# Performance work log

Measured on AMD Instinct MI355X. Metric: run time of the kernel, lower is better.

The kernel has to match this reference:

```python
import jax, jax.numpy as jnp
import numpy as np

B, S, E = 2, 2048, 2048
H, D = 16, 128  # num_attention_heads, head_dim = hidden_size // num_heads


def rotate_half(x):
    x1 = x[..., : x.shape[-1] // 2]
    x2 = x[..., x.shape[-1] // 2 :]
    return jnp.concatenate((-x2, x1), axis=-1)


def setup_inputs() -> dict:
    key = jax.random.key(0)
    ks = jax.random.split(key, 7)
    return {
        "hidden_states": jax.random.normal(ks[0], (B, S, E), dtype=jnp.float32),
        "cos": jax.random.uniform(ks[1], (1, 1, S, D), dtype=jnp.float32),
        "sin": jax.random.uniform(ks[2], (1, 1, S, D), dtype=jnp.float32),
        "wq": jax.random.normal(ks[3], (E, H * D), dtype=jnp.float32) / np.sqrt(E),
        "wk": jax.random.normal(ks[4], (E, H * D), dtype=jnp.float32) / np.sqrt(E),
        "wv": jax.random.normal(ks[5], (E, H * D), dtype=jnp.float32) / np.sqrt(E),
        "wo": jax.random.normal(ks[6], (H * D, E), dtype=jnp.float32) / np.sqrt(H * D),
    }


def reference(hidden_states, cos, sin, wq, wk, wv, wo):
    # QKV projections (no bias, per attention_bias=False)
    q = (hidden_states @ wq).reshape(B, S, H, D).transpose(0, 2, 1, 3)  # bhsd
    k = (hidden_states @ wk).reshape(B, S, H, D).transpose(0, 2, 1, 3)
    v = (hidden_states @ wv).reshape(B, S, H, D).transpose(0, 2, 1, 3)
    # RoPE (applied after the head transpose, as in the original)
    q = q * cos + rotate_half(q) * sin
    k = k * cos + rotate_half(k) * sin
    # NOTE: original forward never applies self.scaling and uses no causal mask.
    scores = jnp.einsum("bhqd,bhkd->bhqk", q, k)
    attn = jax.nn.softmax(scores.astype(jnp.float32), axis=-1)
    out = jnp.einsum("bhqk,bhkd->bhqd", attn, v)
    out = out.transpose(0, 2, 1, 3).reshape(B, S, H * D)
    return out @ wo
```

## Files before the change

### kernel.cpp

```cpp
#include <hip/hip_runtime.h>
#include <stdint.h>

typedef _Float16 f16;
typedef _Float16 half8 __attribute__((ext_vector_type(8)));
typedef _Float16 half4 __attribute__((ext_vector_type(4)));
typedef __fp16 fp16x2 __attribute__((ext_vector_type(2)));
typedef float f32x4 __attribute__((ext_vector_type(4)));
typedef float f32x16 __attribute__((ext_vector_type(16)));
typedef uint32_t u32x4 __attribute__((ext_vector_type(4)));

static constexpr int Bsz = 2, S = 2048, E = 2048, H = 16, D = 128;
static constexpr int M = Bsz * S;
static constexpr int N_QKV = 3 * H * D;
static constexpr int HD = H * D;

__device__ __forceinline__ void gload_lds16(const void* gp, void* lp) {
  __builtin_amdgcn_global_load_lds(
      (const __attribute__((address_space(1))) uint32_t*)(uintptr_t)gp,
      (__attribute__((address_space(3))) uint32_t*)(uint32_t)(uintptr_t)lp,
      16, 0, 0);
}

__device__ __forceinline__ uint32_t pkrtz(float a, float b) {
  fp16x2 r = __builtin_amdgcn_cvt_pkrtz(a, b);
  return __builtin_bit_cast(uint32_t, r);
}

__global__ void cast_f32_f16(const float* __restrict__ in, f16* __restrict__ out) {
  size_t i = (size_t)(blockIdx.x * 256 + threadIdx.x) * 8;
  float4 a = *(const float4*)&in[i];
  float4 b = *(const float4*)&in[i + 4];
  half8 h;
  h[0] = (f16)a.x; h[1] = (f16)a.y; h[2] = (f16)a.z; h[3] = (f16)a.w;
  h[4] = (f16)b.x; h[5] = (f16)b.y; h[6] = (f16)b.z; h[7] = (f16)b.w;
  *(half8*)&out[i] = h;
}

__global__ void transpose_cast(const float* __restrict__ wq, const float* __restrict__ wk,
                               const float* __restrict__ wv, const float* __restrict__ wo,
                               f16* __restrict__ wt, f16* __restrict__ wot) {
  __shared__ float tile[32][33];
  int z = blockIdx.z;
  const float* src = (z == 0) ? wq : (z == 1) ? wk : (z == 2) ? wv : wo;
  f16* dst = (z == 3) ? wot : wt + (size_t)z * E * HD;
  int bx = blockIdx.x * 32, by = blockIdx.y * 32;
  int tx = threadIdx.x, ty = threadIdx.y;
#pragma unroll
  for (int r = 0; r < 4; ++r)
    tile[ty + r * 8][tx] = src[(size_t)(by + ty + r * 8) * 2048 + bx + tx];
  __syncthreads();
#pragma unroll
  for (int r = 0; r < 4; ++r)
    dst[(size_t)(bx + ty + r * 8) * 2048 + by + tx] = (f16)tile[tx][ty + r * 8];
}

#define ABUF(b_, kh_) ((b_) * 16384 + (kh_) * 8192)
#define BBUF(b_) (32768 + (b_) * 16384)
#define STAGE_A(T_, kh_)                                                     \
  do {                                                                       \
    int ko_ = (T_) * 64 + (kh_) * 32;                                        \
    int bb_ = (T_) & 1;                                                      \
    gload_lds16(Abase + ko_ + ca0, &lds[ABUF(bb_, kh_) + t * 8]);            \
    gload_lds16(Abase + ko_ + ca1, &lds[ABUF(bb_, kh_) + 4096 + t * 8]);     \
  } while (0)
#define STAGE_B(T_)                                                          \
  do {                                                                       \
    int ko_ = (T_) * 64;                                                     \
    int bb_ = (T_) & 1;                                                      \
    gload_lds16(Br0 + ko_, &lds[BBUF(bb_) + t * 8]);                         \
    gload_lds16(Br1 + ko_, &lds[BBUF(bb_) + 4096 + t * 8]);                  \
    gload_lds16(Br2 + ko_, &lds[BBUF(bb_) + 8192 + t * 8]);                  \
    gload_lds16(Br3 + ko_, &lds[BBUF(bb_) + 12288 + t * 8]);                 \
  } while (0)
#define LDA4(mh_, kh_)                                                       \
  _Pragma("unroll") for (int i2 = 0; i2 < 4; ++i2) {                         \
    int ra = wm * 128 + ((mh_)*4 + i2) * 16 + lr;                            \
    int s_ = g ^ ((ra >> 2) & 3);                                            \
    af[i2] = *(const half8*)&lds[ABUF(cb, kh_) + (s_ >> 1) * 4096 + ra * 16 + (s_ & 1) * 8]; \
  }
#define LDB4(kh_, RB_)                                                       \
  _Pragma("unroll") for (int j = 0; j < 4; ++j) {                            \
    int rb = (RB_);                                                          \
    bf[j] = *(const half8*)&lds[BBUF(cb) + rb * 64 + ((((kh_)*4) + g) ^ (rb & 7)) * 8]; \
  }
#define MM16(mh_, SWAP_)                                                     \
  __builtin_amdgcn_s_setprio(1);                                             \
  _Pragma("unroll") for (int i2 = 0; i2 < 4; ++i2)                           \
  _Pragma("unroll") for (int j = 0; j < 4; ++j)                              \
      acc[(mh_)*4 + i2][j] = (SWAP_)                                         \
          ? __builtin_amdgcn_mfma_f32_16x16x32_f16(bf[j], af[i2], acc[(mh_)*4 + i2][j], 0, 0, 0) \
          : __builtin_amdgcn_mfma_f32_16x16x32_f16(af[i2], bf[j], acc[(mh_)*4 + i2][j], 0, 0, 0); \
  __builtin_amdgcn_s_setprio(0);
#define BAR() __builtin_amdgcn_s_barrier()
#define VM8() asm volatile("s_waitcnt vmcnt(8)" ::: "memory")
#define VM6() asm volatile("s_waitcnt vmcnt(6)" ::: "memory")
#define VM0() asm volatile("s_waitcnt vmcnt(0)" ::: "memory")
#define KLOOP(RB_, SWAP_)                                                    \
  for (int T = 0; T < 32; ++T) {                                             \
    const int cb = T & 1;                                                    \
    half8 af[4], bf[4];                                                      \
    LDB4(0, RB_); LDA4(0, 0);                                                \
    if (T + 1 < 32) STAGE_A(T + 1, 1);                                       \
    BAR(); MM16(0, SWAP_); BAR();                                            \
    LDA4(1, 0);                                                              \
    if (T >= 29) { VM0(); } else { VM8(); }                                  \
    BAR(); MM16(1, SWAP_); BAR();                                            \
    LDB4(1, RB_); LDA4(0, 1);                                                \
    if (T + 2 < 32) STAGE_A(T + 2, 0);                                       \
    BAR(); MM16(0, SWAP_); BAR();                                            \
    LDA4(1, 1);                                                              \
    if (T + 2 < 32) STAGE_B(T + 2);                                          \
    if (T >= 29) { VM0(); } else { VM8(); }                                  \
    BAR(); MM16(1, SWAP_); BAR();                                            \
  }

__global__ __launch_bounds__(512, 1) void qkv256(const f16* __restrict__ A,
                                                 const f16* __restrict__ Bt,
                                                 const float* __restrict__ cosb,
                                                 const float* __restrict__ sinb,
                                                 f16* __restrict__ Qb,
                                                 f16* __restrict__ Kb,
                                                 f16* __restrict__ VtG) {
  __shared__ f16 lds[65536];
  const int Kk = E;
  const int t = threadIdx.x, l = t & 63, wid = t >> 6;
  const int wm = wid >> 2, wn = wid & 3;
  const int lr = l & 15, g = l >> 4;
  const int bid = blockIdx.x;
  const int bm = (bid & 7) * 2 + ((bid >> 3) & 1);
  const int bn = bid >> 4;
  const int arow = t >> 1, ah = t & 1;
  const int fa = (arow >> 2) & 3;
  const int ca0 = (ah ^ fa) * 8;
  const int ca1 = ((2 | ah) ^ fa) * 8;
  const f16* Abase = A + (size_t)(bm * 256 + arow) * Kk;
  const int brl = t >> 3, bc = t & 7;
  const int cbx = (bc ^ (brl & 7)) * 8;
  const f16* Br0 = Bt + (size_t)(bn * 256 + brl) * Kk + cbx;
  const f16* Br1 = Bt + (size_t)(bn * 256 + 64 + brl) * Kk + cbx;
  const f16* Br2 = Bt + (size_t)(bn * 256 + 128 + brl) * Kk + cbx;
  const f16* Br3 = Bt + (size_t)(bn * 256 + 192 + brl) * Kk + cbx;
  const int bt = bn >> 3;
  const int h0 = (bn & 7) * 2;
  const int b = bm >> 3;
  const int sblk = (bm & 7) * 256;

  f32x4 acc[8][4] = {};
  STAGE_A(0, 0); STAGE_A(0, 1); STAGE_B(0);
  STAGE_A(1, 0); STAGE_B(1);
  VM6();
  BAR();

  if (bt < 2) {
    KLOOP(wn * 16 + ((j & 1) << 6) + ((j >> 1) << 7) + lr, true)
    f16* Dst = (bt == 0) ? Qb : Kb;
#pragma unroll
    for (int mi = 0; mi < 8; ++mi) {
      const int s = sblk + wm * 128 + mi * 16 + lr;
      const size_t cbase = (size_t)s * D;
      const int dlo = wn * 16 + g * 4;
      float4 cl = *(const float4*)&cosb[cbase + dlo];
      float4 ch = *(const float4*)&cosb[cbase + dlo + 64];
      float4 sl = *(const float4*)&sinb[cbase + dlo];
      float4 sh = *(const float4*)&sinb[cbase + dlo + 64];
      float cla[4] = {cl.x, cl.y, cl.z, cl.w}, cha[4] = {ch.x, ch.y, ch.z, ch.w};
      float sla[4] = {sl.x, sl.y, sl.z, sl.w}, sha[4] = {sh.x, sh.y, sh.z, sh.w};
#pragma unroll
      for (int jh = 0; jh < 2; ++jh) {
        const int bh = b * 16 + h0 + jh;
        const size_t obase = ((size_t)bh * S + s) * D;
        half4 olo, ohi;
#pragma unroll
        for (int r = 0; r < 4; ++r) {
          float xl = acc[mi][2 * jh][r], xh = acc[mi][2 * jh + 1][r];
          olo[r] = (f16)(xl * cla[r] - xh * sla[r]);
          ohi[r] = (f16)(xh * cha[r] + xl * sha[r]);
        }
        *(half4*)&Dst[obase + dlo] = olo;
        *(half4*)&Dst[obase + dlo + 64] = ohi;
      }
    }
  } else {
    KLOOP(wn * 64 + j * 16 + lr, false)
#pragma unroll
    for (int j = 0; j < 4; ++j) {
      const int cv = (bn & 7) * 256 + wn * 64 + j * 16 + lr;
      const int h = cv >> 7, d = cv & 127;
      const size_t rowb = ((size_t)(b * 16 + h) * D + d) * S;
#pragma unroll
      for (int mi = 0; mi < 8; ++mi) {
        const int s0 = sblk + wm * 128 + mi * 16 + g * 4;
        half4 h4;
#pragma unroll
        for (int r = 0; r < 4; ++r) h4[r] = (f16)acc[mi][j][r];
        *(half4*)&VtG[rowb + s0] = h4;
      }
    }
  }
}
#undef ABUF
#undef BBUF
#undef STAGE_A
#undef STAGE_B
#undef LDA4
#undef LDB4
#undef MM16
#undef KLOOP
#undef VM8
#undef VM6
#undef VM0
#undef BAR

#define STAGE4(PTR, BASE, KOFF, DST)                                       \
  gload_lds16(&PTR[BASE + (KOFF) + scol], &DST[t * 8]);                    \
  gload_lds16(&PTR[BASE + (size_t)64 * Kk + (KOFF) + scol], &DST[2048 + t * 8]);

template <typename OutT>
__global__ __launch_bounds__(256, 4) void gemm_bt(const f16* __restrict__ A,
                                                  const f16* __restrict__ Bt,
                                                  OutT* __restrict__ C,
                                                  int Nn, int Kk) {
  __shared__ f16 As[8192];
  __shared__ f16 Bs[8192];
  const int t = threadIdx.x, l = t & 63;
  const int wm = (t >> 7) & 1, wn = (t >> 6) & 1;
  const int bid = blockIdx.x;
  const int bm = (bid & 7) * 4 + ((bid >> 3) & 3);
  const int bn = bid >> 5;
  const int lr = l & 15, g = l >> 4;
  const int srow = t >> 2;
  const int scol = (((t & 3) ^ (srow & 3)) * 8);
  const size_t abase = (size_t)(bm * 128 + srow) * Kk;
  const size_t bbase = (size_t)(bn * 128 + srow) * Kk;
  f32x4 acc[4][4] = {};
  for (int k0 = 0; k0 < Kk; k0 += 64) {
    __syncthreads();
    STAGE4(A, abase, k0, As);
    STAGE4(Bt, bbase, k0, Bs);
    STAGE4(A, abase, k0 + 32, (As + 4096));
    STAGE4(Bt, bbase, k0 + 32, (Bs + 4096));
    __syncthreads();
#pragma unroll
    for (int kh = 0; kh < 2; ++kh) {
      const int so = kh * 4096;
      half8 af[4], bf[4];
#pragma unroll
      for (int i = 0; i < 4; ++i) {
        int ra = wm * 64 + i * 16 + lr;
        int rb = wn * 64 + i * 16 + lr;
        af[i] = *(const half8*)&As[so + ra * 32 + ((g ^ (ra & 3)) * 8)];
        bf[i] = *(const half8*)&Bs[so + rb * 32 + ((g ^ (rb & 3)) * 8)];
      }
#pragma unroll
      for (int i = 0; i < 4; ++i)
#pragma unroll
        for (int j = 0; j < 4; ++j)
          acc[i][j] = __builtin_amdgcn_mfma_f32_16x16x32_f16(af[i], bf[j], acc[i][j], 0, 0, 0);
    }
  }
#pragma unroll
  for (int i = 0; i < 4; ++i)
#pragma unroll
    for (int j = 0; j < 4; ++j) {
      int row = bm * 128 + wm * 64 + i * 16 + g * 4;
      int col = bn * 128 + wn * 64 + j * 16 + lr;
#pragma unroll
      for (int r = 0; r < 4; ++r)
        C[(size_t)(row + r) * Nn + col] = (OutT)acc[i][j][r];
    }
}

__device__ __forceinline__ void stage_kv(const f16* __restrict__ Kg, const f16* __restrict__ Vg,
                                         f16* KsB, f16* VsB, int t, int kv) {
#pragma unroll
  for (int rnd = 0; rnd < 4; ++rnd) {
    int row = rnd * 16 + (t >> 4);
    int c = t & 15;
    gload_lds16(&Kg[(size_t)(kv + row) * D + ((c ^ (row & 7)) * 8)], &KsB[rnd * 2048 + t * 8]);
  }
#pragma unroll
  for (int rnd = 0; rnd < 4; ++rnd) {
    int row = rnd * 32 + (t >> 3);
    int c = t & 7;
    gload_lds16(&Vg[(size_t)row * S + kv + ((c ^ (row & 7)) * 8)], &VsB[rnd * 2048 + t * 8]);
  }
}

__global__ __launch_bounds__(256, 2) void flash_attn2(const f16* __restrict__ Q,
                                                      const f16* __restrict__ K,
                                                      const f16* __restrict__ Vt,
                                                      f16* __restrict__ O) {
  __shared__ f16 lds[2][16384];
  const int t = threadIdx.x, l = t & 63, w = t >> 6;
  const int c = l & 31, hi = l >> 5;
  int bid = blockIdx.x;
  bid = (bid & 7) * 64 + (bid >> 3);
  const int bh = bid >> 4, qt = bid & 15;
  const size_t baseQ = (size_t)bh * S * D;
  const f16* Kg = K + baseQ;
  const f16* Vg = Vt + (size_t)bh * D * S;
  const int q0 = qt * 128 + w * 32;
  half8 qf[8];
#pragma unroll
  for (int dc = 0; dc < 8; ++dc)
    qf[dc] = *(const half8*)&Q[baseQ + (size_t)(q0 + c) * D + dc * 16 + hi * 8];
  f32x16 o[4] = {};
  float m = -3.0e38f, ssum = 0.f;

  stage_kv(Kg, Vg, &lds[0][0], &lds[0][8192], t, 0);
  __syncthreads();

  for (int it = 0; it < S / 64; ++it) {
    const int cur = it & 1;
    const f16* KsB = &lds[cur][0];
    const f16* VsB = &lds[cur][8192];
    if (it + 1 < S / 64) stage_kv(Kg, Vg, &lds[cur ^ 1][0], &lds[cur ^ 1][8192], t, (it + 1) * 64);

    f32x16 s0 = {}, s1 = {};
    __builtin_amdgcn_s_setprio(1);
#pragma unroll
    for (int dc = 0; dc < 8; ++dc) {
      const int r0 = c, r1 = 32 + c;
      half8 kf0 = *(const half8*)&KsB[r0 * 128 + (((2 * dc + hi) ^ (r0 & 7)) * 8)];
      half8 kf1 = *(const half8*)&KsB[r1 * 128 + (((2 * dc + hi) ^ (r1 & 7)) * 8)];
      s0 = __builtin_amdgcn_mfma_f32_32x32x16_f16(kf0, qf[dc], s0, 0, 0, 0);
      s1 = __builtin_amdgcn_mfma_f32_32x32x16_f16(kf1, qf[dc], s1, 0, 0, 0);
    }
    __builtin_amdgcn_s_setprio(0);

    float tm = s0[0];
#pragma unroll
    for (int r = 1; r < 16; ++r) tm = fmaxf(tm, s0[r]);
#pragma unroll
    for (int r = 0; r < 16; ++r) tm = fmaxf(tm, s1[r]);
    tm = fmaxf(tm, __shfl_xor(tm, 32));
    if (!__all(tm <= m + 8.f)) {
      float mn = fmaxf(m, tm);
      float corr = __expf(m - mn);
      m = mn;
      ssum *= corr;
#pragma unroll
      for (int dt = 0; dt < 4; ++dt)
#pragma unroll
        for (int r = 0; r < 16; ++r) o[dt][r] *= corr;
    }
    float ts = 0.f;
#pragma unroll
    for (int r = 0; r < 16; ++r) { s0[r] = __expf(s0[r] - m); ts += s0[r]; }
#pragma unroll
    for (int r = 0; r < 16; ++r) { s1[r] = __expf(s1[r] - m); ts += s1[r]; }
    ts += __shfl_xor(ts, 32);
    ssum += ts;

    half8 pf[4];
#pragma unroll
    for (int ks = 0; ks < 4; ++ks) {
      const int B0 = 2 * (ks & 1), B1 = B0 + 1;
      uint32_t X0, X1, Y0, Y1;
      if (ks < 2) {
        X0 = pkrtz(s0[4 * B0 + 0], s0[4 * B0 + 1]);
        X1 = pkrtz(s0[4 * B0 + 2], s0[4 * B0 + 3]);
        Y0 = pkrtz(s0[4 * B1 + 0], s0[4 * B1 + 1]);
        Y1 = pkrtz(s0[4 * B1 + 2], s0[4 * B1 + 3]);
      } else {
        X0 = pkrtz(s1[4 * B0 + 0], s1[4 * B0 + 1]);
        X1 = pkrtz(s1[4 * B0 + 2], s1[4 * B0 + 3]);
        Y0 = pkrtz(s1[4 * B1 + 0], s1[4 * B1 + 1]);
        Y1 = pkrtz(s1[4 * B1 + 2], s1[4 * B1 + 3]);
      }
      asm volatile("v_permlane32_swap_b32 %0, %1" : "+v"(X0), "+v"(Y0));
      asm volatile("v_permlane32_swap_b32 %0, %1" : "+v"(X1), "+v"(Y1));
      u32x4 pw; pw[0] = X0; pw[1] = X1; pw[2] = Y0; pw[3] = Y1;
      pf[ks] = __builtin_bit_cast(half8, pw);
    }

    __builtin_amdgcn_s_setprio(1);
#pragma unroll
    for (int dt = 0; dt < 4; ++dt) {
      const int row = dt * 32 + c;
#pragma unroll
      for (int ks = 0; ks < 4; ++ks) {
        half8 vf = *(const half8*)&VsB[row * 64 + (((2 * ks + hi) ^ (row & 7)) * 8)];
        o[dt] = __builtin_amdgcn_mfma_f32_32x32x16_f16(vf, pf[ks], o[dt], 0, 0, 0);
      }
    }
    __builtin_amdgcn_s_setprio(0);
    __syncthreads();
  }

  const float inv = 1.f / ssum;
  const int b = bh >> 4, h = bh & 15;
  const size_t orow = ((size_t)(b * S + q0 + c)) * HD + h * D;
#pragma unroll
  for (int dt = 0; dt < 4; ++dt)
#pragma unroll
    for (int b2 = 0; b2 < 4; ++b2) {
      half4 h4;
#pragma unroll
      for (int a = 0; a < 4; ++a) h4[a] = (f16)(o[dt][4 * b2 + a] * inv);
      *(half4*)&O[orow + dt * 32 + 8 * b2 + 4 * hi] = h4;
    }
}

extern "C" void kernel_launch(void* const* d_in, const int* in_sizes, int n_in,
                              void* d_out, int out_size, void* d_ws, size_t ws_size,
                              hipStream_t stream) {
  (void)in_sizes; (void)n_in; (void)out_size; (void)ws_size;
  const float* hs = (const float*)d_in[0];
  const float* cosb = (const float*)d_in[1];
  const float* sinb = (const float*)d_in[2];
  const float* wq = (const float*)d_in[3];
  const float* wk = (const float*)d_in[4];
  const float* wv = (const float*)d_in[5];
  const float* wo = (const float*)d_in[6];
  float* out = (float*)d_out;
  char* ws = (char*)d_ws;
  f16* hs16 = (f16*)(ws);
  f16* attn = (f16*)(ws);
  f16* wt   = (f16*)(ws + (16u << 20));
  f16* wot  = (f16*)(ws + (40u << 20));
  f16* Qb   = (f16*)(ws + (48u << 20));
  f16* Kb   = (f16*)(ws + (64u << 20));
  f16* VtG  = (f16*)(ws + (80u << 20));

  cast_f32_f16<<<dim3(4096), dim3(256), 0, stream>>>(hs, hs16);
  transpose_cast<<<dim3(64, 64, 4), dim3(32, 8), 0, stream>>>(wq, wk, wv, wo, wt, wot);
  qkv256<<<dim3(384), dim3(512), 0, stream>>>(hs16, wt, cosb, sinb, Qb, Kb, VtG);
  flash_attn2<<<dim3(512), dim3(256), 0, stream>>>(Qb, Kb, VtG, attn);
  gemm_bt<float><<<dim3(512), dim3(256), 0, stream>>>(attn, wot, out, E, HD);
}
```

Before: 284.6 us.

## Widen QKV GEMM tile to 256x384 and move V transpose to separate kernel

```diff
diff --git a/kernel.cpp b/kernel.cpp
--- a/kernel.cpp
+++ b/kernel.cpp
@@ -55,7 +55,7 @@
 }
 
 #define ABUF(b_, kh_) ((b_) * 16384 + (kh_) * 8192)
-#define BBUF(b_) (32768 + (b_) * 16384)
+#define BBUF(kh_) (32768 + (kh_) * 12288)
 #define STAGE_A(T_, kh_)                                                     \
   do {                                                                       \
     int ko_ = (T_) * 64 + (kh_) * 32;                                        \
@@ -63,14 +63,12 @@
     gload_lds16(Abase + ko_ + ca0, &lds[ABUF(bb_, kh_) + t * 8]);            \
     gload_lds16(Abase + ko_ + ca1, &lds[ABUF(bb_, kh_) + 4096 + t * 8]);     \
   } while (0)
-#define STAGE_B(T_)                                                          \
+#define STAGE_B(T_, kh_)                                                     \
   do {                                                                       \
-    int ko_ = (T_) * 64;                                                     \
-    int bb_ = (T_) & 1;                                                      \
-    gload_lds16(Br0 + ko_, &lds[BBUF(bb_) + t * 8]);                         \
-    gload_lds16(Br1 + ko_, &lds[BBUF(bb_) + 4096 + t * 8]);                  \
-    gload_lds16(Br2 + ko_, &lds[BBUF(bb_) + 8192 + t * 8]);                  \
-    gload_lds16(Br3 + ko_, &lds[BBUF(bb_) + 12288 + t * 8]);                 \
+    int ko_ = (T_) * 64 + (kh_) * 32;                                        \
+    gload_lds16(Bb0 + ko_, &lds[BBUF(kh_) + t * 8]);                         \
+    gload_lds16(Bb1 + ko_, &lds[BBUF(kh_) + 4096 + t * 8]);                  \
+    gload_lds16(Bb2 + ko_, &lds[BBUF(kh_) + 8192 + t * 8]);                  \
   } while (0)
 #define LDA4(mh_, kh_)                                                       \
   _Pragma("unroll") for (int i2 = 0; i2 < 4; ++i2) {                         \
@@ -78,122 +76,115 @@
     int s_ = g ^ ((ra >> 2) & 3);                                            \
     af[i2] = *(const half8*)&lds[ABUF(cb, kh_) + (s_ >> 1) * 4096 + ra * 16 + (s_ & 1) * 8]; \
   }
-#define LDB4(kh_, RB_)                                                       \
-  _Pragma("unroll") for (int j = 0; j < 4; ++j) {                            \
-    int rb = (RB_);                                                          \
-    bf[j] = *(const half8*)&lds[BBUF(cb) + rb * 64 + ((((kh_)*4) + g) ^ (rb & 7)) * 8]; \
-  }
-#define MM16(mh_, SWAP_)                                                     \
+#define LDB6(kh_)                                                            \
+  _Pragma("unroll") for (int j = 0; j < 6; ++j) {                            \
+    int rb = (j >> 1) * 128 + wn * 16 + (j & 1) * 64 + lr;                   \
+    bf[j] = *(const half8*)&lds[BBUF(kh_) + rb * 32 + ((g ^ (rb & 3)) * 8)]; \
+  }
+#define MM24(mh_)                                                            \
   __builtin_amdgcn_s_setprio(1);                                             \
   _Pragma("unroll") for (int i2 = 0; i2 < 4; ++i2)                           \
-  _Pragma("unroll") for (int j = 0; j < 4; ++j)                              \
-      acc[(mh_)*4 + i2][j] = (SWAP_)                                         \
-          ? __builtin_amdgcn_mfma_f32_16x16x32_f16(bf[j], af[i2], acc[(mh_)*4 + i2][j], 0, 0, 0) \
-          : __builtin_amdgcn_mfma_f32_16x16x32_f16(af[i2], bf[j], acc[(mh_)*4 + i2][j], 0, 0, 0); \
+  _Pragma("unroll") for (int j = 0; j < 6; ++j)                              \
+      acc[(mh_)*4 + i2][j] =                                                 \
+          __builtin_amdgcn_mfma_f32_16x16x32_f16(bf[j], af[i2], acc[(mh_)*4 + i2][j], 0, 0, 0); \
   __builtin_amdgcn_s_setprio(0);
 #define BAR() __builtin_amdgcn_s_barrier()
-#define VM8() asm volatile("s_waitcnt vmcnt(8)" ::: "memory")
-#define VM6() asm volatile("s_waitcnt vmcnt(6)" ::: "memory")
+#define VM5() asm volatile("s_waitcnt vmcnt(5)" ::: "memory")
+#define VM3() asm volatile("s_waitcnt vmcnt(3)" ::: "memory")
 #define VM0() asm volatile("s_waitcnt vmcnt(0)" ::: "memory")
-#define KLOOP(RB_, SWAP_)                                                    \
-  for (int T = 0; T < 32; ++T) {                                             \
-    const int cb = T & 1;                                                    \
-    half8 af[4], bf[4];                                                      \
-    LDB4(0, RB_); LDA4(0, 0);                                                \
-    if (T + 1 < 32) STAGE_A(T + 1, 1);                                       \
-    BAR(); MM16(0, SWAP_); BAR();                                            \
-    LDA4(1, 0);                                                              \
-    if (T >= 29) { VM0(); } else { VM8(); }                                  \
-    BAR(); MM16(1, SWAP_); BAR();                                            \
-    LDB4(1, RB_); LDA4(0, 1);                                                \
-    if (T + 2 < 32) STAGE_A(T + 2, 0);                                       \
-    BAR(); MM16(0, SWAP_); BAR();                                            \
-    LDA4(1, 1);                                                              \
-    if (T + 2 < 32) STAGE_B(T + 2);                                          \
-    if (T >= 29) { VM0(); } else { VM8(); }                                  \
-    BAR(); MM16(1, SWAP_); BAR();                                            \
-  }
-
-__global__ __launch_bounds__(512, 1) void qkv256(const f16* __restrict__ A,
+
+__global__ __launch_bounds__(512, 1) void qkv384(const f16* __restrict__ A,
                                                  const f16* __restrict__ Bt,
                                                  const float* __restrict__ cosb,
                                                  const float* __restrict__ sinb,
                                                  f16* __restrict__ Qb,
                                                  f16* __restrict__ Kb,
-                                                 f16* __restrict__ VtG) {
-  __shared__ f16 lds[65536];
+                                                 f16* __restrict__ Vb) {
+  __shared__ f16 lds[57344];
   const int Kk = E;
   const int t = threadIdx.x, l = t & 63, wid = t >> 6;
   const int wm = wid >> 2, wn = wid & 3;
   const int lr = l & 15, g = l >> 4;
   const int bid = blockIdx.x;
-  const int bm = (bid & 7) * 2 + ((bid >> 3) & 1);
-  const int bn = bid >> 4;
+  const int idx = bid >> 3;
+  const int bm = (bid & 7) * 2 + (idx & 1);
+  const int bn = idx >> 1;
   const int arow = t >> 1, ah = t & 1;
   const int fa = (arow >> 2) & 3;
   const int ca0 = (ah ^ fa) * 8;
   const int ca1 = ((2 | ah) ^ fa) * 8;
   const f16* Abase = A + (size_t)(bm * 256 + arow) * Kk;
-  const int brl = t >> 3, bc = t & 7;
-  const int cbx = (bc ^ (brl & 7)) * 8;
-  const f16* Br0 = Bt + (size_t)(bn * 256 + brl) * Kk + cbx;
-  const f16* Br1 = Bt + (size_t)(bn * 256 + 64 + brl) * Kk + cbx;
-  const f16* Br2 = Bt + (size_t)(bn * 256 + 128 + brl) * Kk + cbx;
-  const f16* Br3 = Bt + (size_t)(bn * 256 + 192 + brl) * Kk + cbx;
-  const int bt = bn >> 3;
-  const int h0 = (bn & 7) * 2;
+  const int brow = t >> 2, bch = t & 3;
+  const int cb0 = ((bch ^ (brow & 3)) * 8);
+  const f16* Bb0 = Bt + (size_t)(bn * 384 + brow) * Kk + cb0;
+  const f16* Bb1 = Bt + (size_t)(bn * 384 + 128 + brow) * Kk + cb0;
+  const f16* Bb2 = Bt + (size_t)(bn * 384 + 256 + brow) * Kk + cb0;
   const int b = bm >> 3;
   const int sblk = (bm & 7) * 256;
 
-  f32x4 acc[8][4] = {};
-  STAGE_A(0, 0); STAGE_A(0, 1); STAGE_B(0);
-  STAGE_A(1, 0); STAGE_B(1);
-  VM6();
+  f32x4 acc[8][6] = {};
+  STAGE_A(0, 0); STAGE_A(0, 1);
+  STAGE_B(0, 0); STAGE_B(0, 1);
+  VM3();
   BAR();
 
-  if (bt < 2) {
-    KLOOP(wn * 16 + ((j & 1) << 6) + ((j >> 1) << 7) + lr, true)
-    f16* Dst = (bt == 0) ? Qb : Kb;
-#pragma unroll
-    for (int mi = 0; mi < 8; ++mi) {
-      const int s = sblk + wm * 128 + mi * 16 + lr;
-      const size_t cbase = (size_t)s * D;
-      const int dlo = wn * 16 + g * 4;
-      float4 cl = *(const float4*)&cosb[cbase + dlo];
-      float4 ch = *(const float4*)&cosb[cbase + dlo + 64];
-      float4 sl = *(const float4*)&sinb[cbase + dlo];
-      float4 sh = *(const float4*)&sinb[cbase + dlo + 64];
-      float cla[4] = {cl.x, cl.y, cl.z, cl.w}, cha[4] = {ch.x, ch.y, ch.z, ch.w};
-      float sla[4] = {sl.x, sl.y, sl.z, sl.w}, sha[4] = {sh.x, sh.y, sh.z, sh.w};
-#pragma unroll
-      for (int jh = 0; jh < 2; ++jh) {
-        const int bh = b * 16 + h0 + jh;
-        const size_t obase = ((size_t)bh * S + s) * D;
+  for (int T = 0; T < 32; ++T) {
+    const int cb = T & 1;
+    half8 af[4], bf[6];
+    LDB6(0); LDA4(0, 0);
+    if (T + 1 < 32) STAGE_A(T + 1, 1);
+    BAR(); MM24(0); BAR();
+    LDA4(1, 0);
+    if (T + 1 < 32) STAGE_B(T + 1, 0);
+    if (T == 31) { VM0(); } else { VM5(); }
+    BAR(); MM24(1); BAR();
+    LDB6(1); LDA4(0, 1);
+    if (T + 1 < 32) STAGE_A(T + 1, 0);
+    BAR(); MM24(0); BAR();
+    LDA4(1, 1);
+    if (T + 1 < 32) STAGE_B(T + 1, 1);
+    if (T == 31) { VM0(); } else { VM3(); }
+    BAR(); MM24(1); BAR();
+  }
+
+  const int dlo = wn * 16 + g * 4;
+#pragma unroll
+  for (int mi = 0; mi < 8; ++mi) {
+    const int s = sblk + wm * 128 + mi * 16 + lr;
+    const size_t cbase = (size_t)s * D;
+    float4 cl = *(const float4*)&cosb[cbase + dlo];
+    float4 ch = *(const float4*)&cosb[cbase + dlo + 64];
+    float4 sl = *(const float4*)&sinb[cbase + dlo];
+    float4 sh = *(const float4*)&sinb[cbase + dlo + 64];
+    float cla[4] = {cl.x, cl.y, cl.z, cl.w}, cha[4] = {ch.x, ch.y, ch.z, ch.w};
+    float sla[4] = {sl.x, sl.y, sl.z, sl.w}, sha[4] = {sh.x, sh.y, sh.z, sh.w};
+#pragma unroll
+    for (int a = 0; a < 3; ++a) {
+      const int n128 = bn * 384 + a * 128;
+      const int region = n128 >> 11;
+      const int h = (n128 >> 7) & 15;
+      const int bh = b * 16 + h;
+      const size_t obase = ((size_t)bh * S + s) * D;
+      if (region < 2) {
+        f16* Dst = (region == 0) ? Qb : Kb;
         half4 olo, ohi;
 #pragma unroll
         for (int r = 0; r < 4; ++r) {
-          float xl = acc[mi][2 * jh][r], xh = acc[mi][2 * jh + 1][r];
+          float xl = acc[mi][2 * a][r], xh = acc[mi][2 * a + 1][r];
           olo[r] = (f16)(xl * cla[r] - xh * sla[r]);
           ohi[r] = (f16)(xh * cha[r] + xl * sha[r]);
         }
         *(half4*)&Dst[obase + dlo] = olo;
         *(half4*)&Dst[obase + dlo + 64] = ohi;
-      }
-    }
-  } else {
-    KLOOP(wn * 64 + j * 16 + lr, false)
-#pragma unroll
-    for (int j = 0; j < 4; ++j) {
-      const int cv = (bn & 7) * 256 + wn * 64 + j * 16 + lr;
-      const int h = cv >> 7, d = cv & 127;
-      const size_t rowb = ((size_t)(b * 16 + h) * D + d) * S;
-#pragma unroll
-      for (int mi = 0; mi < 8; ++mi) {
-        const int s0 = sblk + wm * 128 + mi * 16 + g * 4;
-        half4 h4;
-#pragma unroll
-        for (int r = 0; r < 4; ++r) h4[r] = (f16)acc[mi][j][r];
-        *(half4*)&VtG[rowb + s0] = h4;
+      } else {
+        half4 vlo, vhi;
+#pragma unroll
+        for (int r = 0; r < 4; ++r) {
+          vlo[r] = (f16)acc[mi][2 * a][r];
+          vhi[r] = (f16)acc[mi][2 * a + 1][r];
+        }
+        *(half4*)&Vb[obase + dlo] = vlo;
+        *(half4*)&Vb[obase + dlo + 64] = vhi;
       }
     }
   }
@@ -203,13 +194,37 @@
 #undef STAGE_A
 #undef STAGE_B
 #undef LDA4
-#undef LDB4
-#undef MM16
-#undef KLOOP
-#undef VM8
-#undef VM6
+#undef LDB6
+#undef MM24
+#undef VM5
+#undef VM3
 #undef VM0
 #undef BAR
+
+__global__ void transpose_v(const f16* __restrict__ Vb, f16* __restrict__ VtG) {
+  __shared__ f16 tl[64][136];
+  int bid = blockIdx.x;
+  int bh = bid >> 5, st = bid & 31;
+  int t = threadIdx.x;
+  int s0 = st * 64;
+#pragma unroll
+  for (int rnd = 0; rnd < 4; ++rnd) {
+    int row = rnd * 16 + (t >> 4);
+    int ch = t & 15;
+    half8 v = *(const half8*)&Vb[((size_t)bh * S + s0 + row) * D + ch * 8];
+    *(half8*)&tl[row][ch * 8] = v;
+  }
+  __syncthreads();
+#pragma unroll
+  for (int rnd = 0; rnd < 4; ++rnd) {
+    int d = rnd * 32 + (t >> 3);
+    int ch = t & 7;
+    half8 v;
+#pragma unroll
+    for (int j = 0; j < 8; ++j) v[j] = tl[ch * 8 + j][d];
+    *(half8*)&VtG[((size_t)bh * D + d) * S + s0 + ch * 8] = v;
+  }
+}
 
 #define STAGE4(PTR, BASE, KOFF, DST)                                       \
   gload_lds16(&PTR[BASE + (KOFF) + scol], &DST[t * 8]);                    \
@@ -422,10 +437,12 @@
   f16* Qb   = (f16*)(ws + (48u << 20));
   f16* Kb   = (f16*)(ws + (64u << 20));
   f16* VtG  = (f16*)(ws + (80u << 20));
+  f16* Vb   = (f16*)(ws + (96u << 20));
 
   cast_f32_f16<<<dim3(4096), dim3(256), 0, stream>>>(hs, hs16);
   transpose_cast<<<dim3(64, 64, 4), dim3(32, 8), 0, stream>>>(wq, wk, wv, wo, wt, wot);
-  qkv256<<<dim3(384), dim3(512), 0, stream>>>(hs16, wt, cosb, sinb, Qb, Kb, VtG);
+  qkv384<<<dim3(256), dim3(512), 0, stream>>>(hs16, wt, cosb, sinb, Qb, Kb, Vb);
+  transpose_v<<<dim3(1024), dim3(256), 0, stream>>>(Vb, VtG);
   flash_attn2<<<dim3(512), dim3(256), 0, stream>>>(Qb, Kb, VtG, attn);
   gemm_bt<float><<<dim3(512), dim3(256), 0, stream>>>(attn, wot, out, E, HD);
 }
```

Measured after the change: 323.0 us. 1.13x slower.
